# Kernel optimization log

Hardware: AMD Instinct MI355X
Metric: run time of the kernel (lower is better)

Reference implementation:

```python
import jax, jax.numpy as jnp
import numpy as np

N = 50000      # nodes
DEG = 16       # fixed neighbor count per node -> E = N*DEG edges
F_IN = 128
F_OUT = 128


def setup_inputs() -> dict:
    key = jax.random.key(0)
    k = jax.random.split(key, 6)
    E = N * DEG
    x = jax.random.normal(k[0], (N, F_IN), dtype=jnp.float32)
    weight = jax.random.normal(k[1], (F_IN, F_OUT), dtype=jnp.float32) * (1.0 / np.sqrt(F_OUT))
    bias = jax.random.normal(k[2], (F_OUT,), dtype=jnp.float32) * (1.0 / np.sqrt(F_OUT))
    weights_mask = jax.random.normal(k[3], (2 * F_IN, F_IN), dtype=jnp.float32) * (1.0 / np.sqrt(F_IN))
    adj_vals = jax.random.uniform(k[4], (E,), dtype=jnp.float32)
    edge_src = jax.random.randint(k[5], (E,), 0, N, dtype=jnp.int32)   # neighbor ids (add_all flattened)
    edge_dst = jnp.repeat(jnp.arange(N, dtype=jnp.int32), DEG)         # center node ids
    return {"x": x, "weight": weight, "bias": bias, "weights_mask": weights_mask,
            "adj_vals": adj_vals, "edge_src": edge_src, "edge_dst": edge_dst}


def reference(x, weight, bias, weights_mask, adj_vals, edge_src, edge_dst):
    # Per-edge: concat(center, neighbor) -> mask MLP -> sigmoid (dropout omitted: eval mode)
    cen = x[edge_dst]                    # [E, F]
    nei = x[edge_src]                    # [E, F]
    cen_nei = jnp.concatenate([cen, nei], axis=1)          # [E, 2F]
    mask = jax.nn.sigmoid(cen_nei @ weights_mask)          # [E, F]
    # Weighted neighbor sum scattered back to centers, plus self feature
    agg = jax.ops.segment_sum(mask * nei, edge_dst, num_segments=N)   # [N, F]
    x_new = x + agg
    # Dense transform then spmm aggregation (adj given as edge list with values)
    support = x_new @ weight                                # [N, F_out]
    out = jax.ops.segment_sum(adj_vals[:, None] * support[edge_src], edge_dst, num_segments=N)
    return out + bias
```

## Files before the change

kernel.cpp:

```cpp
#include <hip/hip_runtime.h>
#include <stdint.h>
#include <stddef.h>


#define NNODES 50000
#define DEG    16
#define FD     128

#define NEG_LOG2E -1.44269504f

typedef __bf16 bf16x8 __attribute__((ext_vector_type(8)));
typedef short  s16x8  __attribute__((ext_vector_type(8)));
typedef float  f32x4  __attribute__((ext_vector_type(4)));
typedef float  f32x2  __attribute__((ext_vector_type(2)));

__device__ __forceinline__ short f2bf_s(float f) {
    union { float f; uint32_t u; } v; v.f = f;
    uint32_t r = v.u + 0x7fffu + ((v.u >> 16) & 1u);
    return (short)(r >> 16);
}
__device__ __forceinline__ float bflo(uint32_t u) {
    union { uint32_t u; float f; } v; v.u = u << 16;
    return v.f;
}
__device__ __forceinline__ float bfhi(uint32_t u) {
    union { uint32_t u; float f; } v; v.u = u & 0xffff0000u;
    return v.f;
}

__global__ __launch_bounds__(256) void pack_k(const float* __restrict__ wm,
                                              const float* __restrict__ w,
                                              short* __restrict__ wmb,
                                              short* __restrict__ wpack) {
    int tid = blockIdx.x * 256 + threadIdx.x;
    if (tid < 128 * 256) {
        int k = tid >> 8, c = tid & 255;
        float v = (c < 128) ? wm[k * 128 + c] : wm[(128 + k) * 128 + (c - 128)];
        int idx = (((k >> 5) * 16 + (c >> 4)) * 64 + ((k >> 3) & 3) * 16 + (c & 15)) * 8 + (k & 7);
        wmb[idx] = f2bf_s(NEG_LOG2E * v);
    }
    if (tid < 128 * 128) {
        int k = tid >> 7, n = tid & 127;
        int idx = (((k >> 5) * 8 + (n >> 4)) * 64 + ((k >> 3) & 3) * 16 + (n & 15)) * 8 + (k & 7);
        wpack[idx] = f2bf_s(w[tid]);
    }
}

__global__ __launch_bounds__(256) void zy_k(const float* __restrict__ x,
                                            const short* __restrict__ wmb,
                                            short* __restrict__ zbf,
                                            uint32_t* __restrict__ xb,
                                            uint8_t* __restrict__ y8) {
    __shared__ float ct[16 * 260];
    const int tid = threadIdx.x, wave = tid >> 6, lane = tid & 63;
    const int q = lane >> 4, m = lane & 15;
    const int node0 = blockIdx.x * 16;

    f32x4 acc[4];
    #pragma unroll
    for (int nt = 0; nt < 4; ++nt) acc[nt] = (f32x4){0.f, 0.f, 0.f, 0.f};

    #pragma unroll
    for (int kk = 0; kk < 4; ++kk) {
        const float* rp = x + (size_t)(node0 + m) * FD + kk * 32 + q * 8;
        f32x4 lo = *reinterpret_cast<const f32x4*>(rp);
        f32x4 hi = *reinterpret_cast<const f32x4*>(rp + 4);
        bf16x8 a;
        a[0]=(__bf16)lo.x; a[1]=(__bf16)lo.y; a[2]=(__bf16)lo.z; a[3]=(__bf16)lo.w;
        a[4]=(__bf16)hi.x; a[5]=(__bf16)hi.y; a[6]=(__bf16)hi.z; a[7]=(__bf16)hi.w;
        #pragma unroll
        for (int nt = 0; nt < 4; ++nt) {
            int frag = kk * 16 + wave * 4 + nt;
            s16x8 braw = *reinterpret_cast<const s16x8*>(wmb + ((size_t)frag * 64 + lane) * 8);
            acc[nt] = __builtin_amdgcn_mfma_f32_16x16x32_bf16(a, __builtin_bit_cast(bf16x8, braw), acc[nt], 0, 0, 0);
        }
    }
    #pragma unroll
    for (int nt = 0; nt < 4; ++nt)
        #pragma unroll
        for (int i = 0; i < 4; ++i)
            ct[(q * 4 + i) * 260 + wave * 64 + nt * 16 + m] = acc[nt][i];
    __syncthreads();

    const int row = tid >> 4;
    const int c0  = (tid & 15) * 16;
    const int grow = node0 + row;
    if (c0 < 128) {
        uint32_t zo[8];
        #pragma unroll
        for (int j = 0; j < 8; ++j) {
            float v0 = ct[row * 260 + c0 + 2 * j];
            float v1 = ct[row * 260 + c0 + 2 * j + 1];
            zo[j] = (uint32_t)(uint16_t)f2bf_s(v0) | ((uint32_t)(uint16_t)f2bf_s(v1) << 16);
        }
        uint4* dst = reinterpret_cast<uint4*>(zbf + (size_t)grow * FD + c0);
        dst[0] = make_uint4(zo[0], zo[1], zo[2], zo[3]);
        dst[1] = make_uint4(zo[4], zo[5], zo[6], zo[7]);
    } else {
        const int f0 = c0 - 128;
        const float* xr = x + (size_t)grow * FD + f0;
        uint32_t xo[8];
        #pragma unroll
        for (int j = 0; j < 8; ++j) {
            float v0 = xr[2 * j], v1 = xr[2 * j + 1];
            xo[j] = (uint32_t)(uint16_t)f2bf_s(v0) | ((uint32_t)(uint16_t)f2bf_s(v1) << 16);
        }
        uint4* xdst = reinterpret_cast<uint4*>(xb + (size_t)grow * 64 + f0 / 2);
        xdst[0] = make_uint4(xo[0], xo[1], xo[2], xo[3]);
        xdst[1] = make_uint4(xo[4], xo[5], xo[6], xo[7]);
        uint32_t yo[4];
        #pragma unroll
        for (int g = 0; g < 4; ++g) {
            float y0 = ct[row * 260 + c0 + 4 * g];
            float y1 = ct[row * 260 + c0 + 4 * g + 1];
            float y2 = ct[row * 260 + c0 + 4 * g + 2];
            float y3 = ct[row * 260 + c0 + 4 * g + 3];
            int u = __builtin_amdgcn_cvt_pk_fp8_f32(y0, y1, 0, false);
            u     = __builtin_amdgcn_cvt_pk_fp8_f32(y2, y3, u, true);
            yo[g] = (uint32_t)u;
        }
        *reinterpret_cast<uint4*>(y8 + (size_t)grow * 128 + f0) = make_uint4(yo[0], yo[1], yo[2], yo[3]);
    }
}

__global__ __launch_bounds__(256) void edge_k(const short* __restrict__ zbf,
                                              const uint32_t* __restrict__ xb,
                                              const uint8_t* __restrict__ y8,
                                              const int* __restrict__ esrc,
                                              uint32_t* __restrict__ xnb) {
    const int tid = threadIdx.x, wave = tid >> 6, lane = tid & 63;
    const int wn0 = blockIdx.x * 16 + wave * 4;

    #pragma unroll
    for (int pr = 0; pr < 2; ++pr) {
        const int nuA = __builtin_amdgcn_readfirstlane(wn0 + pr * 2);
        const int nuB = __builtin_amdgcn_readfirstlane(wn0 + pr * 2 + 1);
        const int* epA = esrc + nuA * DEG;
        const int* epB = esrc + nuB * DEG;
        uint32_t zA = reinterpret_cast<const uint32_t*>(zbf + (size_t)nuA * FD)[lane];
        uint32_t zB = reinterpret_cast<const uint32_t*>(zbf + (size_t)nuB * FD)[lane];
        uint32_t cAw = xb[(size_t)nuA * 64 + lane];
        uint32_t cBw = xb[(size_t)nuB * 64 + lane];
        const float zA0 = bflo(zA), zA1 = bfhi(zA);
        const float zB0 = bflo(zB), zB1 = bfhi(zB);
        float aA0 = 0.f, aA1 = 0.f, bA0 = 0.f, bA1 = 0.f;
        float aB0 = 0.f, aB1 = 0.f, bB0 = 0.f, bB1 = 0.f;
        #pragma unroll
        for (int e = 0; e < 16; ++e) {
            const int sA = epA[e], sB = epB[e];
            uint32_t xA = xb[(size_t)sA * 64 + lane];
            uint32_t xB = xb[(size_t)sB * 64 + lane];
            uint32_t yA = *reinterpret_cast<const uint16_t*>(y8 + (size_t)sA * 128 + 2 * lane);
            uint32_t yB = *reinterpret_cast<const uint16_t*>(y8 + (size_t)sB * 128 + 2 * lane);
            f32x2 pA = __builtin_amdgcn_cvt_pk_f32_fp8((int)yA, false);
            f32x2 pB = __builtin_amdgcn_cvt_pk_f32_fp8((int)yB, false);
            float gA0 = __builtin_amdgcn_rcpf(1.f + __builtin_amdgcn_exp2f(zA0 + pA.x));
            float gA1 = __builtin_amdgcn_rcpf(1.f + __builtin_amdgcn_exp2f(zA1 + pA.y));
            float gB0 = __builtin_amdgcn_rcpf(1.f + __builtin_amdgcn_exp2f(zB0 + pB.x));
            float gB1 = __builtin_amdgcn_rcpf(1.f + __builtin_amdgcn_exp2f(zB1 + pB.y));
            if (e & 1) { bA0 += gA0 * bflo(xA); bA1 += gA1 * bfhi(xA); bB0 += gB0 * bflo(xB); bB1 += gB1 * bfhi(xB); }
            else       { aA0 += gA0 * bflo(xA); aA1 += gA1 * bfhi(xA); aB0 += gB0 * bflo(xB); aB1 += gB1 * bfhi(xB); }
        }
        float xA0 = bflo(cAw) + aA0 + bA0, xA1 = bfhi(cAw) + aA1 + bA1;
        float xB0 = bflo(cBw) + aB0 + bB0, xB1 = bfhi(cBw) + aB1 + bB1;
        xnb[(size_t)nuA * 64 + lane] = (uint32_t)(uint16_t)f2bf_s(xA0) | ((uint32_t)(uint16_t)f2bf_s(xA1) << 16);
        xnb[(size_t)nuB * 64 + lane] = (uint32_t)(uint16_t)f2bf_s(xB0) | ((uint32_t)(uint16_t)f2bf_s(xB1) << 16);
    }
}

__global__ __launch_bounds__(256) void out_k(const uint32_t* __restrict__ xnb,
                                             const float* __restrict__ adj,
                                             const int* __restrict__ esrc,
                                             const short* __restrict__ wpack,
                                             const float* __restrict__ bias,
                                             float* __restrict__ out) {
    __shared__ float xn[16 * 132];
    const int tid = threadIdx.x, wave = tid >> 6, lane = tid & 63;
    const int q = lane >> 4, m = lane & 15;
    const int node0 = blockIdx.x * 16;
    const int wn0 = node0 + wave * 4;

    #pragma unroll
    for (int pr = 0; pr < 2; ++pr) {
        const int nuA = __builtin_amdgcn_readfirstlane(wn0 + pr * 2);
        const int nuB = __builtin_amdgcn_readfirstlane(wn0 + pr * 2 + 1);
        const int* epA = esrc + nuA * DEG;
        const int* epB = esrc + nuB * DEG;
        const float* apA = adj + nuA * DEG;
        const float* apB = adj + nuB * DEG;
        float aA0 = 0.f, aA1 = 0.f, bA0 = 0.f, bA1 = 0.f;
        float aB0 = 0.f, aB1 = 0.f, bB0 = 0.f, bB1 = 0.f;
        #pragma unroll
        for (int e = 0; e < 16; ++e) {
            uint32_t uA = xnb[(size_t)epA[e] * 64 + lane];
            uint32_t uB = xnb[(size_t)epB[e] * 64 + lane];
            float wA = apA[e], wB = apB[e];
            if (e & 1) { bA0 += wA * bflo(uA); bA1 += wA * bfhi(uA); bB0 += wB * bflo(uB); bB1 += wB * bfhi(uB); }
            else       { aA0 += wA * bflo(uA); aA1 += wA * bfhi(uA); aB0 += wB * bflo(uB); aB1 += wB * bfhi(uB); }
        }
        const int rA = wave * 4 + pr * 2, rB = rA + 1;
        f32x2 tA; tA.x = aA0 + bA0; tA.y = aA1 + bA1;
        f32x2 tB; tB.x = aB0 + bB0; tB.y = aB1 + bB1;
        *reinterpret_cast<f32x2*>(&xn[rA * 132 + 2 * lane]) = tA;
        *reinterpret_cast<f32x2*>(&xn[rB * 132 + 2 * lane]) = tB;
    }
    __syncthreads();

    f32x4 sacc[2];
    sacc[0] = (f32x4){0.f, 0.f, 0.f, 0.f};
    sacc[1] = (f32x4){0.f, 0.f, 0.f, 0.f};
    #pragma unroll
    for (int kk = 0; kk < 4; ++kk) {
        const float* p = &xn[m * 132 + kk * 32 + q * 8];
        bf16x8 a;
        a[0]=(__bf16)p[0]; a[1]=(__bf16)p[1]; a[2]=(__bf16)p[2]; a[3]=(__bf16)p[3];
        a[4]=(__bf16)p[4]; a[5]=(__bf16)p[5]; a[6]=(__bf16)p[6]; a[7]=(__bf16)p[7];
        #pragma unroll
        for (int t = 0; t < 2; ++t) {
            int nt = wave * 2 + t;
            s16x8 braw = *reinterpret_cast<const s16x8*>(wpack + ((size_t)(kk * 8 + nt) * 64 + lane) * 8);
            sacc[t] = __builtin_amdgcn_mfma_f32_16x16x32_bf16(a, __builtin_bit_cast(bf16x8, braw), sacc[t], 0, 0, 0);
        }
    }
    #pragma unroll
    for (int t = 0; t < 2; ++t) {
        const int f = (wave * 2 + t) * 16 + m;
        const float bv = bias[f];
        #pragma unroll
        for (int i = 0; i < 4; ++i)
            out[(size_t)(node0 + q * 4 + i) * FD + f] = sacc[t][i] + bv;
    }
}

extern "C" void kernel_launch(void* const* d_in, const int* in_sizes, int n_in,
                              void* d_out, int out_size, void* d_ws, size_t ws_size,
                              hipStream_t stream) {
    const float* x      = (const float*)d_in[0];
    const float* weight = (const float*)d_in[1];
    const float* bias   = (const float*)d_in[2];
    const float* wm     = (const float*)d_in[3];
    const float* adj    = (const float*)d_in[4];
    const int*   esrc   = (const int*)d_in[5];

    short*    wmb   = (short*)d_ws;
    short*    wpack = (short*)((char*)d_ws + 65536);
    short*    zbf   = (short*)((char*)d_ws + 98304);
    uint32_t* xnb   = (uint32_t*)((char*)d_ws + 98304 + (size_t)NNODES * FD * 2);
    uint32_t* xb    = (uint32_t*)d_out;
    uint8_t*  y8    = (uint8_t*)d_out + (size_t)NNODES * FD * 2;
    float*    out   = (float*)d_out;

    pack_k <<<128,         256, 0, stream>>>(wm, weight, wmb, wpack);
    zy_k   <<<NNODES / 16, 256, 0, stream>>>(x, wmb, zbf, xb, y8);
    edge_k <<<NNODES / 16, 256, 0, stream>>>(zbf, xb, y8, esrc, xnb);
    out_k  <<<NNODES / 16, 256, 0, stream>>>(xnb, adj, esrc, wpack, bias, out);
}
```

Before: 180.2 us.

## Precompute exp factors per node and restructure gathers to wide per-quarter-wave loads

The exponentials are moved into zy_k, which now stores exp2 of the center and neighbor logits, so the per-edge sigmoid becomes rcp(1 + Ez*Ey) and exp2 leaves the edge loop. Both edge_k and out_k now map one node to each quarter-wave, with each lane owning 8 features. All 16 neighbor indices are loaded as int4 and all 16 row gathers are issued as wide uint4/uint2 loads before any arithmetic. The aim is to cut per-edge transcendental work and raise memory-level parallelism in the gathers. The cost is precision: storing exp values in bf16 and fp8 risks overflow or underflow for large logits (fp8 e4m3 has a small range), and holding 16 wide loads in flight raises register pressure.

```diff
diff --git a/kernel.cpp b/kernel.cpp
--- a/kernel.cpp
+++ b/kernel.cpp
@@ -26,6 +26,9 @@
 __device__ __forceinline__ float bfhi(uint32_t u) {
     union { uint32_t u; float f; } v; v.u = u & 0xffff0000u;
     return v.f;
+}
+__device__ __forceinline__ uint32_t pkbf(float lo, float hi) {
+    return (uint32_t)(uint16_t)f2bf_s(lo) | ((uint32_t)(uint16_t)f2bf_s(hi) << 16);
 }
 
 __global__ __launch_bounds__(256) void pack_k(const float* __restrict__ wm,
@@ -48,7 +51,7 @@
 
 __global__ __launch_bounds__(256) void zy_k(const float* __restrict__ x,
                                             const short* __restrict__ wmb,
-                                            short* __restrict__ zbf,
+                                            short* __restrict__ ezb,
                                             uint32_t* __restrict__ xb,
                                             uint8_t* __restrict__ y8) {
     __shared__ float ct[16 * 260];
@@ -89,11 +92,11 @@
         uint32_t zo[8];
         #pragma unroll
         for (int j = 0; j < 8; ++j) {
-            float v0 = ct[row * 260 + c0 + 2 * j];
-            float v1 = ct[row * 260 + c0 + 2 * j + 1];
-            zo[j] = (uint32_t)(uint16_t)f2bf_s(v0) | ((uint32_t)(uint16_t)f2bf_s(v1) << 16);
-        }
-        uint4* dst = reinterpret_cast<uint4*>(zbf + (size_t)grow * FD + c0);
+            float v0 = __builtin_amdgcn_exp2f(ct[row * 260 + c0 + 2 * j]);
+            float v1 = __builtin_amdgcn_exp2f(ct[row * 260 + c0 + 2 * j + 1]);
+            zo[j] = pkbf(v0, v1);
+        }
+        uint4* dst = reinterpret_cast<uint4*>(ezb + (size_t)grow * FD + c0);
         dst[0] = make_uint4(zo[0], zo[1], zo[2], zo[3]);
         dst[1] = make_uint4(zo[4], zo[5], zo[6], zo[7]);
     } else {
@@ -103,7 +106,7 @@
         #pragma unroll
         for (int j = 0; j < 8; ++j) {
             float v0 = xr[2 * j], v1 = xr[2 * j + 1];
-            xo[j] = (uint32_t)(uint16_t)f2bf_s(v0) | ((uint32_t)(uint16_t)f2bf_s(v1) << 16);
+            xo[j] = pkbf(v0, v1);
         }
         uint4* xdst = reinterpret_cast<uint4*>(xb + (size_t)grow * 64 + f0 / 2);
         xdst[0] = make_uint4(xo[0], xo[1], xo[2], xo[3]);
@@ -111,10 +114,10 @@
         uint32_t yo[4];
         #pragma unroll
         for (int g = 0; g < 4; ++g) {
-            float y0 = ct[row * 260 + c0 + 4 * g];
-            float y1 = ct[row * 260 + c0 + 4 * g + 1];
-            float y2 = ct[row * 260 + c0 + 4 * g + 2];
-            float y3 = ct[row * 260 + c0 + 4 * g + 3];
+            float y0 = __builtin_amdgcn_exp2f(ct[row * 260 + c0 + 4 * g]);
+            float y1 = __builtin_amdgcn_exp2f(ct[row * 260 + c0 + 4 * g + 1]);
+            float y2 = __builtin_amdgcn_exp2f(ct[row * 260 + c0 + 4 * g + 2]);
+            float y3 = __builtin_amdgcn_exp2f(ct[row * 260 + c0 + 4 * g + 3]);
             int u = __builtin_amdgcn_cvt_pk_fp8_f32(y0, y1, 0, false);
             u     = __builtin_amdgcn_cvt_pk_fp8_f32(y2, y3, u, true);
             yo[g] = (uint32_t)u;
@@ -123,49 +126,61 @@
     }
 }
 
-__global__ __launch_bounds__(256) void edge_k(const short* __restrict__ zbf,
+__global__ __launch_bounds__(256) void edge_k(const short* __restrict__ ezb,
                                               const uint32_t* __restrict__ xb,
                                               const uint8_t* __restrict__ y8,
                                               const int* __restrict__ esrc,
                                               uint32_t* __restrict__ xnb) {
     const int tid = threadIdx.x, wave = tid >> 6, lane = tid & 63;
-    const int wn0 = blockIdx.x * 16 + wave * 4;
-
-    #pragma unroll
-    for (int pr = 0; pr < 2; ++pr) {
-        const int nuA = __builtin_amdgcn_readfirstlane(wn0 + pr * 2);
-        const int nuB = __builtin_amdgcn_readfirstlane(wn0 + pr * 2 + 1);
-        const int* epA = esrc + nuA * DEG;
-        const int* epB = esrc + nuB * DEG;
-        uint32_t zA = reinterpret_cast<const uint32_t*>(zbf + (size_t)nuA * FD)[lane];
-        uint32_t zB = reinterpret_cast<const uint32_t*>(zbf + (size_t)nuB * FD)[lane];
-        uint32_t cAw = xb[(size_t)nuA * 64 + lane];
-        uint32_t cBw = xb[(size_t)nuB * 64 + lane];
-        const float zA0 = bflo(zA), zA1 = bfhi(zA);
-        const float zB0 = bflo(zB), zB1 = bfhi(zB);
-        float aA0 = 0.f, aA1 = 0.f, bA0 = 0.f, bA1 = 0.f;
-        float aB0 = 0.f, aB1 = 0.f, bB0 = 0.f, bB1 = 0.f;
-        #pragma unroll
-        for (int e = 0; e < 16; ++e) {
-            const int sA = epA[e], sB = epB[e];
-            uint32_t xA = xb[(size_t)sA * 64 + lane];
-            uint32_t xB = xb[(size_t)sB * 64 + lane];
-            uint32_t yA = *reinterpret_cast<const uint16_t*>(y8 + (size_t)sA * 128 + 2 * lane);
-            uint32_t yB = *reinterpret_cast<const uint16_t*>(y8 + (size_t)sB * 128 + 2 * lane);
-            f32x2 pA = __builtin_amdgcn_cvt_pk_f32_fp8((int)yA, false);
-            f32x2 pB = __builtin_amdgcn_cvt_pk_f32_fp8((int)yB, false);
-            float gA0 = __builtin_amdgcn_rcpf(1.f + __builtin_amdgcn_exp2f(zA0 + pA.x));
-            float gA1 = __builtin_amdgcn_rcpf(1.f + __builtin_amdgcn_exp2f(zA1 + pA.y));
-            float gB0 = __builtin_amdgcn_rcpf(1.f + __builtin_amdgcn_exp2f(zB0 + pB.x));
-            float gB1 = __builtin_amdgcn_rcpf(1.f + __builtin_amdgcn_exp2f(zB1 + pB.y));
-            if (e & 1) { bA0 += gA0 * bflo(xA); bA1 += gA1 * bfhi(xA); bB0 += gB0 * bflo(xB); bB1 += gB1 * bfhi(xB); }
-            else       { aA0 += gA0 * bflo(xA); aA1 += gA1 * bfhi(xA); aB0 += gB0 * bflo(xB); aB1 += gB1 * bfhi(xB); }
-        }
-        float xA0 = bflo(cAw) + aA0 + bA0, xA1 = bfhi(cAw) + aA1 + bA1;
-        float xB0 = bflo(cBw) + aB0 + bB0, xB1 = bfhi(cBw) + aB1 + bB1;
-        xnb[(size_t)nuA * 64 + lane] = (uint32_t)(uint16_t)f2bf_s(xA0) | ((uint32_t)(uint16_t)f2bf_s(xA1) << 16);
-        xnb[(size_t)nuB * 64 + lane] = (uint32_t)(uint16_t)f2bf_s(xB0) | ((uint32_t)(uint16_t)f2bf_s(xB1) << 16);
-    }
+    const int q = lane >> 4, li = lane & 15;
+    const int n0 = __builtin_amdgcn_readfirstlane(blockIdx.x * 16 + wave * 4);
+    const int nd = n0 + q;
+
+    const int4* ep = reinterpret_cast<const int4*>(esrc + nd * DEG);
+    const int4 s0 = ep[0], s1 = ep[1], s2 = ep[2], s3 = ep[3];
+
+    const uint4 ez = *reinterpret_cast<const uint4*>(
+        reinterpret_cast<const uint32_t*>(ezb) + (size_t)nd * 64 + li * 4);
+    const uint4 cw = *reinterpret_cast<const uint4*>(xb + (size_t)nd * 64 + li * 4);
+
+    uint4 xw0, xw1, xw2, xw3, xw4, xw5, xw6, xw7, xw8, xw9, xw10, xw11, xw12, xw13, xw14, xw15;
+    uint2 yw0, yw1, yw2, yw3, yw4, yw5, yw6, yw7, yw8, yw9, yw10, yw11, yw12, yw13, yw14, yw15;
+#define LD(I, S) \
+    xw##I = *reinterpret_cast<const uint4*>(xb + (size_t)(S) * 64 + li * 4); \
+    yw##I = *reinterpret_cast<const uint2*>(y8 + (size_t)(S) * 128 + li * 8);
+    LD(0, s0.x)  LD(1, s0.y)  LD(2, s0.z)  LD(3, s0.w)
+    LD(4, s1.x)  LD(5, s1.y)  LD(6, s1.z)  LD(7, s1.w)
+    LD(8, s2.x)  LD(9, s2.y)  LD(10, s2.z) LD(11, s2.w)
+    LD(12, s3.x) LD(13, s3.y) LD(14, s3.z) LD(15, s3.w)
+#undef LD
+
+    const float Ez0 = bflo(ez.x), Ez1 = bfhi(ez.x), Ez2 = bflo(ez.y), Ez3 = bfhi(ez.y),
+                Ez4 = bflo(ez.z), Ez5 = bfhi(ez.z), Ez6 = bflo(ez.w), Ez7 = bfhi(ez.w);
+    float a0 = 0.f, a1 = 0.f, a2 = 0.f, a3 = 0.f, a4 = 0.f, a5 = 0.f, a6 = 0.f, a7 = 0.f;
+#define ACC(I) { \
+    f32x2 p0 = __builtin_amdgcn_cvt_pk_f32_fp8((int)yw##I.x, false); \
+    f32x2 p1 = __builtin_amdgcn_cvt_pk_f32_fp8((int)yw##I.x, true);  \
+    f32x2 p2 = __builtin_amdgcn_cvt_pk_f32_fp8((int)yw##I.y, false); \
+    f32x2 p3 = __builtin_amdgcn_cvt_pk_f32_fp8((int)yw##I.y, true);  \
+    a0 = __builtin_fmaf(__builtin_amdgcn_rcpf(__builtin_fmaf(Ez0, p0.x, 1.f)), bflo(xw##I.x), a0); \
+    a1 = __builtin_fmaf(__builtin_amdgcn_rcpf(__builtin_fmaf(Ez1, p0.y, 1.f)), bfhi(xw##I.x), a1); \
+    a2 = __builtin_fmaf(__builtin_amdgcn_rcpf(__builtin_fmaf(Ez2, p1.x, 1.f)), bflo(xw##I.y), a2); \
+    a3 = __builtin_fmaf(__builtin_amdgcn_rcpf(__builtin_fmaf(Ez3, p1.y, 1.f)), bfhi(xw##I.y), a3); \
+    a4 = __builtin_fmaf(__builtin_amdgcn_rcpf(__builtin_fmaf(Ez4, p2.x, 1.f)), bflo(xw##I.z), a4); \
+    a5 = __builtin_fmaf(__builtin_amdgcn_rcpf(__builtin_fmaf(Ez5, p2.y, 1.f)), bfhi(xw##I.z), a5); \
+    a6 = __builtin_fmaf(__builtin_amdgcn_rcpf(__builtin_fmaf(Ez6, p3.x, 1.f)), bflo(xw##I.w), a6); \
+    a7 = __builtin_fmaf(__builtin_amdgcn_rcpf(__builtin_fmaf(Ez7, p3.y, 1.f)), bfhi(xw##I.w), a7); }
+    ACC(0)  ACC(1)  ACC(2)  ACC(3)
+    ACC(4)  ACC(5)  ACC(6)  ACC(7)
+    ACC(8)  ACC(9)  ACC(10) ACC(11)
+    ACC(12) ACC(13) ACC(14) ACC(15)
+#undef ACC
+
+    const uint32_t o0 = pkbf(bflo(cw.x) + a0, bfhi(cw.x) + a1);
+    const uint32_t o1 = pkbf(bflo(cw.y) + a2, bfhi(cw.y) + a3);
+    const uint32_t o2 = pkbf(bflo(cw.z) + a4, bfhi(cw.z) + a5);
+    const uint32_t o3 = pkbf(bflo(cw.w) + a6, bfhi(cw.w) + a7);
+    *reinterpret_cast<uint4*>(xnb + (size_t)nd * 64 + li * 4) = make_uint4(o0, o1, o2, o3);
 }
 
 __global__ __launch_bounds__(256) void out_k(const uint32_t* __restrict__ xnb,
@@ -177,33 +192,39 @@
     __shared__ float xn[16 * 132];
     const int tid = threadIdx.x, wave = tid >> 6, lane = tid & 63;
     const int q = lane >> 4, m = lane & 15;
+    const int li = m;
     const int node0 = blockIdx.x * 16;
-    const int wn0 = node0 + wave * 4;
-
-    #pragma unroll
-    for (int pr = 0; pr < 2; ++pr) {
-        const int nuA = __builtin_amdgcn_readfirstlane(wn0 + pr * 2);
-        const int nuB = __builtin_amdgcn_readfirstlane(wn0 + pr * 2 + 1);
-        const int* epA = esrc + nuA * DEG;
-        const int* epB = esrc + nuB * DEG;
-        const float* apA = adj + nuA * DEG;
-        const float* apB = adj + nuB * DEG;
-        float aA0 = 0.f, aA1 = 0.f, bA0 = 0.f, bA1 = 0.f;
-        float aB0 = 0.f, aB1 = 0.f, bB0 = 0.f, bB1 = 0.f;
-        #pragma unroll
-        for (int e = 0; e < 16; ++e) {
-            uint32_t uA = xnb[(size_t)epA[e] * 64 + lane];
-            uint32_t uB = xnb[(size_t)epB[e] * 64 + lane];
-            float wA = apA[e], wB = apB[e];
-            if (e & 1) { bA0 += wA * bflo(uA); bA1 += wA * bfhi(uA); bB0 += wB * bflo(uB); bB1 += wB * bfhi(uB); }
-            else       { aA0 += wA * bflo(uA); aA1 += wA * bfhi(uA); aB0 += wB * bflo(uB); aB1 += wB * bfhi(uB); }
-        }
-        const int rA = wave * 4 + pr * 2, rB = rA + 1;
-        f32x2 tA; tA.x = aA0 + bA0; tA.y = aA1 + bA1;
-        f32x2 tB; tB.x = aB0 + bB0; tB.y = aB1 + bB1;
-        *reinterpret_cast<f32x2*>(&xn[rA * 132 + 2 * lane]) = tA;
-        *reinterpret_cast<f32x2*>(&xn[rB * 132 + 2 * lane]) = tB;
-    }
+    const int n0 = __builtin_amdgcn_readfirstlane(node0 + wave * 4);
+    const int nd = n0 + q;
+
+    const int4* ep = reinterpret_cast<const int4*>(esrc + nd * DEG);
+    const int4 s0 = ep[0], s1 = ep[1], s2 = ep[2], s3 = ep[3];
+    const float4* ap = reinterpret_cast<const float4*>(adj + nd * DEG);
+    const float4 w0 = ap[0], w1 = ap[1], w2 = ap[2], w3 = ap[3];
+
+    uint4 u0, u1, u2, u3, u4, u5, u6, u7, u8, u9, u10, u11, u12, u13, u14, u15;
+#define LD(I, S) u##I = *reinterpret_cast<const uint4*>(xnb + (size_t)(S) * 64 + li * 4);
+    LD(0, s0.x)  LD(1, s0.y)  LD(2, s0.z)  LD(3, s0.w)
+    LD(4, s1.x)  LD(5, s1.y)  LD(6, s1.z)  LD(7, s1.w)
+    LD(8, s2.x)  LD(9, s2.y)  LD(10, s2.z) LD(11, s2.w)
+    LD(12, s3.x) LD(13, s3.y) LD(14, s3.z) LD(15, s3.w)
+#undef LD
+
+    float a0 = 0.f, a1 = 0.f, a2 = 0.f, a3 = 0.f, a4 = 0.f, a5 = 0.f, a6 = 0.f, a7 = 0.f;
+#define ACC(I, W) \
+    a0 = __builtin_fmaf(W, bflo(u##I.x), a0); a1 = __builtin_fmaf(W, bfhi(u##I.x), a1); \
+    a2 = __builtin_fmaf(W, bflo(u##I.y), a2); a3 = __builtin_fmaf(W, bfhi(u##I.y), a3); \
+    a4 = __builtin_fmaf(W, bflo(u##I.z), a4); a5 = __builtin_fmaf(W, bfhi(u##I.z), a5); \
+    a6 = __builtin_fmaf(W, bflo(u##I.w), a6); a7 = __builtin_fmaf(W, bfhi(u##I.w), a7);
+    ACC(0, w0.x)  ACC(1, w0.y)  ACC(2, w0.z)  ACC(3, w0.w)
+    ACC(4, w1.x)  ACC(5, w1.y)  ACC(6, w1.z)  ACC(7, w1.w)
+    ACC(8, w2.x)  ACC(9, w2.y)  ACC(10, w2.z) ACC(11, w2.w)
+    ACC(12, w3.x) ACC(13, w3.y) ACC(14, w3.z) ACC(15, w3.w)
+#undef ACC
+
+    const int r = wave * 4 + q;
+    *reinterpret_cast<f32x4*>(&xn[r * 132 + li * 8])     = (f32x4){a0, a1, a2, a3};
+    *reinterpret_cast<f32x4*>(&xn[r * 132 + li * 8 + 4]) = (f32x4){a4, a5, a6, a7};
     __syncthreads();
 
     f32x4 sacc[2];
@@ -244,14 +265,14 @@
 
     short*    wmb   = (short*)d_ws;
     short*    wpack = (short*)((char*)d_ws + 65536);
-    short*    zbf   = (short*)((char*)d_ws + 98304);
+    short*    ezb   = (short*)((char*)d_ws + 98304);
     uint32_t* xnb   = (uint32_t*)((char*)d_ws + 98304 + (size_t)NNODES * FD * 2);
     uint32_t* xb    = (uint32_t*)d_out;
     uint8_t*  y8    = (uint8_t*)d_out + (size_t)NNODES * FD * 2;
     float*    out   = (float*)d_out;
 
     pack_k <<<128,         256, 0, stream>>>(wm, weight, wmb, wpack);
-    zy_k   <<<NNODES / 16, 256, 0, stream>>>(x, wmb, zbf, xb, y8);
-    edge_k <<<NNODES / 16, 256, 0, stream>>>(zbf, xb, y8, esrc, xnb);
+    zy_k   <<<NNODES / 16, 256, 0, stream>>>(x, wmb, ezb, xb, y8);
+    edge_k <<<NNODES / 16, 256, 0, stream>>>(ezb, xb, y8, esrc, xnb);
     out_k  <<<NNODES / 16, 256, 0, stream>>>(xnb, adj, esrc, wpack, bias, out);
 }
```

Result: no change. 181.5 us (+0.7%).
